# Optimization experiments

Hardware: AMD Instinct MI355X
Metric: run time of the kernel (lower is better)

## Reference

```python
import jax, jax.numpy as jnp
import numpy as np

P, Q, R, H1, H2, PH, B = 32, 32, 8, 128, 64, 16, 8192
PAIRS = P * Q
OUT = PAIRS * R  # X_Z_layer output units


def _pairwise_mask(p, q, r):
    # rows i*q+k correspond to pair (x_i, z_k): connected to x_i and z_k only
    mx = np.zeros((p * q, p), np.float32)
    for i in range(p):
        mx[i * q:(i + 1) * q, i] = 1.0
    mz = np.tile(np.eye(q, dtype=np.float32), (p, 1))
    m = np.concatenate([mx, mz], axis=1)          # [p*q, p+q]
    return np.repeat(m, r, axis=0)                 # [p*q*r, p+q]


def setup_inputs() -> dict:
    key = jax.random.key(0)
    ks = jax.random.split(key, 24)
    rn = lambda k, s, sc=0.1: jax.random.normal(k, s, jnp.float32) * sc
    x = jax.random.normal(ks[0], (B, P), jnp.float32)
    z = jax.random.normal(ks[1], (B, Q), jnp.float32)
    # X_mlp: P -> H1 -> H2 -> 1
    xw1, xb1 = rn(ks[2], (P, H1)), rn(ks[3], (H1,))
    xw2, xb2 = rn(ks[4], (H1, H2)), rn(ks[5], (H2,))
    xw3, xb3 = rn(ks[6], (H2, 1)), rn(ks[7], (1,))
    # Z_mlp: Q -> H1 -> H2 -> 1
    zw1, zb1 = rn(ks[8], (Q, H1)), rn(ks[9], (H1,))
    zw2, zb2 = rn(ks[10], (Q if False else H1, H2)), rn(ks[11], (H2,))
    zw3, zb3 = rn(ks[12], (H2, 1)), rn(ks[13], (1,))
    # masked X_Z_layer: weight pre-multiplied by structured mask (as in __init__)
    mask = jnp.asarray(_pairwise_mask(P, Q, R))    # [OUT, P+Q]
    xzw = (rn(ks[14], (OUT, P + Q)) * mask).T      # [P+Q, OUT]
    xzb = rn(ks[15], (OUT,))
    # 1024 tiny per-pair MLPs: R -> PH (bias) -> 1 (no bias), stacked
    pw1 = rn(ks[16], (PAIRS, R, PH))
    pb1 = rn(ks[17], (PAIRS, PH))
    pw2 = rn(ks[18], (PAIRS, PH))
    return dict(x=x, z=z, xw1=xw1, xb1=xb1, xw2=xw2, xb2=xb2, xw3=xw3, xb3=xb3,
                zw1=zw1, zb1=zb1, zw2=zw2, zb2=zb2, zw3=zw3, zb3=zb3,
                xzw=xzw, xzb=xzb, pw1=pw1, pb1=pb1, pw2=pw2)


def reference(x, z, xw1, xb1, xw2, xb2, xw3, xb3,
              zw1, zb1, zw2, zb2, zw3, zb3, xzw, xzb, pw1, pb1, pw2):
    relu = jax.nn.relu
    # main-effect MLPs
    hx = relu(relu(x @ xw1 + xb1) @ xw2 + xb2)
    out_x = hx @ xw3 + xb3                         # [B,1]
    hz = relu(relu(z @ zw1 + zb1) @ zw2 + zb2)
    out_z = hz @ zw3 + zb3                         # [B,1]
    # masked interaction layer
    xz = jnp.concatenate([x, z], axis=1)           # [B, P+Q]
    h = relu(xz @ xzw + xzb)                       # [B, OUT]
    # all 1024 per-pair MLPs as one batched GEMM
    hp = h.reshape(h.shape[0], PAIRS, R)           # [B, pairs, R]
    t = relu(jnp.einsum('bpr,prh->bph', hp, pw1) + pb1)
    out_xz = jnp.einsum('bph,ph->b', t, pw2)[:, None]  # sum over pairs -> [B,1]
    return out_x + out_z + out_xz
```

## Files before the change

### kernel.cpp

```cpp
#include <hip/hip_runtime.h>

#define B_TOT 8192
#define PP 32
#define QQ 32
#define RR 8
#define H1 128
#define H2 64
#define PHH 16
#define PAIRS 1024
#define OUT_UNITS 8192

#define NBLK_IA 4096
#define NBLK_MM 512

typedef float f32x16 __attribute__((ext_vector_type(16)));
typedef short s16x8  __attribute__((ext_vector_type(8)));

union FragU { s16x8 v; unsigned int u[4]; };

__device__ inline unsigned int pack_bf16(float lo, float hi) {
    return __builtin_amdgcn_perm(__float_as_uint(hi), __float_as_uint(lo), 0x07060302u);
}

union SharedU {
    union {
        struct {
            float zT[16][128];
            float4 lwx[16][2];
            float4 lwz[16][2];
            float4 lhb[16][2];
            unsigned lpw1[16][4][16];
            float lpb[16][16];
            float lpw2[16][16];
        } s;
        float red[128][33];
    } ia;
    struct {
        float h1T[64][65];
        float red2[4][64];
    } mm;
};

__global__ __launch_bounds__(256, 4) void fused_k(
    const float* __restrict__ x, const float* __restrict__ z,
    const float* __restrict__ xw1, const float* __restrict__ xb1,
    const float* __restrict__ xw2, const float* __restrict__ xb2,
    const float* __restrict__ xw3, const float* __restrict__ xb3,
    const float* __restrict__ zw1, const float* __restrict__ zb1,
    const float* __restrict__ zw2, const float* __restrict__ zb2,
    const float* __restrict__ zw3, const float* __restrict__ zb3,
    const float* __restrict__ xzw, const float* __restrict__ xzb,
    const float* __restrict__ pw1, const float* __restrict__ pb1,
    const float* __restrict__ pw2, float* __restrict__ out)
{
    __shared__ SharedU sh;
    const int bid  = blockIdx.x;
    const int t    = threadIdx.x;
    const int w    = t >> 6;
    const int lane = t & 63;

    if (bid >= NBLK_MM) {
        const int ib    = bid - NBLK_MM;
        const int bx    = ib & 63;
        const int y     = ib >> 6;
        const int m     = lane & 31;
        const int kh    = lane >> 5;
        const int jj    = m & 15;
        const int cph   = m >> 4;
        const int b0    = bx * 128;
        const int i_x   = y >> 1;
        const int k0    = (y & 1) * 16;
        const int pair0 = y * 16;

        {
            int row = t >> 1;
            int c8  = (t & 1) * 8;
            const float* src = z + (size_t)(b0 + row) * 32 + k0 + c8;
            float4 a4 = *reinterpret_cast<const float4*>(src);
            float4 b4 = *reinterpret_cast<const float4*>(src + 4);
            sh.ia.s.zT[c8+0][row] = a4.x; sh.ia.s.zT[c8+1][row] = a4.y;
            sh.ia.s.zT[c8+2][row] = a4.z; sh.ia.s.zT[c8+3][row] = a4.w;
            sh.ia.s.zT[c8+4][row] = b4.x; sh.ia.s.zT[c8+5][row] = b4.y;
            sh.ia.s.zT[c8+6][row] = b4.z; sh.ia.s.zT[c8+7][row] = b4.w;
        }
        if (t < 128) {
            int p = t >> 3, c = t & 7;
            int gp = pair0 + p;
            reinterpret_cast<float*>(sh.ia.s.lwx)[t] = xzw[(size_t)i_x * OUT_UNITS + gp*8 + c];
            reinterpret_cast<float*>(sh.ia.s.lwz)[t] = xzw[(size_t)(32 + k0 + p) * OUT_UNITS + gp*8 + c];
            reinterpret_cast<float*>(sh.ia.s.lhb)[t] = xzb[gp*8 + c];
        }
        {
            int p = t >> 4, j = t & 15;
            int gp = pair0 + p;
            sh.ia.s.lpb[p][j]  = pb1[gp*PHH + j];
            sh.ia.s.lpw2[p][j] = pw2[gp*PHH + j];
        }
        #pragma unroll
        for (int it = 0; it < 4; ++it) {
            int idx = t + it * 256;
            int p = idx >> 6, u = (idx >> 4) & 3, j = idx & 15;
            int gp = pair0 + p;
            float lo = pw1[(size_t)gp * 128 + (2*u)*16 + j];
            float hi = pw1[(size_t)gp * 128 + (2*u+1)*16 + j];
            sh.ia.s.lpw1[p][u][j] = pack_bf16(lo, hi);
        }

        const int bl = (w & 1) * 64 + m;
        const float xv0 = x[(size_t)(b0 + bl)      * 32 + i_x];
        const float xv1 = x[(size_t)(b0 + bl + 32) * 32 + i_x];
        __syncthreads();

        f32x16 acc0, acc1;
        #pragma unroll
        for (int r = 0; r < 16; ++r) { acc0[r] = 0.f; acc1[r] = 0.f; }

        const bool realB = (kh == cph);
        const int  ppl0  = (w >> 1) * 4;

        #pragma unroll 2
        for (int kk = 0; kk < 4; ++kk) {
            const int ppl = ppl0 + kk;
            const int pAl = 2*ppl + kh;
            const int pBl = 2*ppl + cph;

            const float zv0 = sh.ia.s.zT[pAl][bl];
            const float zv1 = sh.ia.s.zT[pAl][bl + 32];
            const float4 wxa = sh.ia.s.lwx[pAl][0], wxb = sh.ia.s.lwx[pAl][1];
            const float4 wza = sh.ia.s.lwz[pAl][0], wzb = sh.ia.s.lwz[pAl][1];
            const float4 hba = sh.ia.s.lhb[pAl][0], hbb = sh.ia.s.lhb[pAl][1];

            float h0[8], h1v[8];
            h0[0] = fmaxf(fmaf(xv0, wxa.x, fmaf(zv0, wza.x, hba.x)), 0.f);
            h0[1] = fmaxf(fmaf(xv0, wxa.y, fmaf(zv0, wza.y, hba.y)), 0.f);
            h0[2] = fmaxf(fmaf(xv0, wxa.z, fmaf(zv0, wza.z, hba.z)), 0.f);
            h0[3] = fmaxf(fmaf(xv0, wxa.w, fmaf(zv0, wza.w, hba.w)), 0.f);
            h0[4] = fmaxf(fmaf(xv0, wxb.x, fmaf(zv0, wzb.x, hbb.x)), 0.f);
            h0[5] = fmaxf(fmaf(xv0, wxb.y, fmaf(zv0, wzb.y, hbb.y)), 0.f);
            h0[6] = fmaxf(fmaf(xv0, wxb.z, fmaf(zv0, wzb.z, hbb.z)), 0.f);
            h0[7] = fmaxf(fmaf(xv0, wxb.w, fmaf(zv0, wzb.w, hbb.w)), 0.f);
            h1v[0] = fmaxf(fmaf(xv1, wxa.x, fmaf(zv1, wza.x, hba.x)), 0.f);
            h1v[1] = fmaxf(fmaf(xv1, wxa.y, fmaf(zv1, wza.y, hba.y)), 0.f);
            h1v[2] = fmaxf(fmaf(xv1, wxa.z, fmaf(zv1, wza.z, hba.z)), 0.f);
            h1v[3] = fmaxf(fmaf(xv1, wxa.w, fmaf(zv1, wza.w, hba.w)), 0.f);
            h1v[4] = fmaxf(fmaf(xv1, wxb.x, fmaf(zv1, wzb.x, hbb.x)), 0.f);
            h1v[5] = fmaxf(fmaf(xv1, wxb.y, fmaf(zv1, wzb.y, hbb.y)), 0.f);
            h1v[6] = fmaxf(fmaf(xv1, wxb.z, fmaf(zv1, wzb.z, hbb.z)), 0.f);
            h1v[7] = fmaxf(fmaf(xv1, wxb.w, fmaf(zv1, wzb.w, hbb.w)), 0.f);

            FragU a0, a1, bf;
            a0.u[0] = pack_bf16(h0[0], h0[1]);
            a0.u[1] = pack_bf16(h0[2], h0[3]);
            a0.u[2] = pack_bf16(h0[4], h0[5]);
            a0.u[3] = pack_bf16(h0[6], h0[7]);
            a1.u[0] = pack_bf16(h1v[0], h1v[1]);
            a1.u[1] = pack_bf16(h1v[2], h1v[3]);
            a1.u[2] = pack_bf16(h1v[4], h1v[5]);
            a1.u[3] = pack_bf16(h1v[6], h1v[7]);
            bf.u[0] = realB ? sh.ia.s.lpw1[pBl][0][jj] : 0u;
            bf.u[1] = realB ? sh.ia.s.lpw1[pBl][1][jj] : 0u;
            bf.u[2] = realB ? sh.ia.s.lpw1[pBl][2][jj] : 0u;
            bf.u[3] = realB ? sh.ia.s.lpw1[pBl][3][jj] : 0u;

            const float pbv = sh.ia.s.lpb[pBl][jj];
            const float w2v = sh.ia.s.lpw2[pBl][jj];

            f32x16 cpb;
            #pragma unroll
            for (int r = 0; r < 16; ++r) cpb[r] = pbv;

            f32x16 d0 = __builtin_amdgcn_mfma_f32_32x32x16_bf16(a0.v, bf.v, cpb, 0, 0, 0);
            f32x16 d1 = __builtin_amdgcn_mfma_f32_32x32x16_bf16(a1.v, bf.v, cpb, 0, 0, 0);

            #pragma unroll
            for (int r = 0; r < 16; ++r)
                acc0[r] = fmaf(fmaxf(d0[r], 0.f), w2v, acc0[r]);
            #pragma unroll
            for (int r = 0; r < 16; ++r)
                acc1[r] = fmaf(fmaxf(d1[r], 0.f), w2v, acc1[r]);
        }

        __syncthreads();
        const int rb0 = (w & 1) * 64;
        if (w < 2) {
            #pragma unroll
            for (int r = 0; r < 16; ++r) {
                int rowf = (r & 3) + 8 * (r >> 2) + 4 * kh;
                sh.ia.red[rb0 + rowf][m]      = acc0[r];
                sh.ia.red[rb0 + 32 + rowf][m] = acc1[r];
            }
        }
        __syncthreads();
        if (w >= 2) {
            #pragma unroll
            for (int r = 0; r < 16; ++r) {
                int rowf = (r & 3) + 8 * (r >> 2) + 4 * kh;
                sh.ia.red[rb0 + rowf][m]      += acc0[r];
                sh.ia.red[rb0 + 32 + rowf][m] += acc1[r];
            }
        }
        __syncthreads();
        if (t < 128) {
            float s = 0.f;
            #pragma unroll
            for (int c = 0; c < 32; ++c) s += sh.ia.red[t][c];
            atomicAdd(out + b0 + t, s);
        }
    } else {
        const int r2    = bid;
        const int btile = r2 & 127;
        const int hf    = (r2 >> 7) & 1;
        const int which = (r2 >> 8) & 1;
        const float* in = which ? z   : x;
        const float* w1 = which ? zw1 : xw1;
        const float* b1 = which ? zb1 : xb1;
        const float* w2 = which ? zw2 : xw2;
        const float* b2 = which ? zb2 : xb2;
        const float* w3 = which ? zw3 : xw3;
        const float* b3 = which ? zb3 : xb3;

        const int wu = __builtin_amdgcn_readfirstlane(w);
        const int b0 = btile * 64;

        float xr[32];
        const float4* xrp = reinterpret_cast<const float4*>(in + (size_t)(b0 + lane) * 32);
        #pragma unroll
        for (int q = 0; q < 8; ++q) {
            float4 v = xrp[q];
            xr[4*q] = v.x; xr[4*q+1] = v.y; xr[4*q+2] = v.z; xr[4*q+3] = v.w;
        }

        const int n0 = __builtin_amdgcn_readfirstlane(hf*32 + wu*8);
        float h2[8];
        #pragma unroll
        for (int n = 0; n < 8; ++n) h2[n] = b2[n0 + n];

        #pragma unroll
        for (int half = 0; half < 2; ++half) {
            const int j0 = half*64 + wu*16;
            float h1[16];
            #pragma unroll
            for (int j = 0; j < 16; ++j) h1[j] = b1[j0 + j];
            #pragma unroll
            for (int mm = 0; mm < 32; ++mm) {
                float xv = xr[mm];
                #pragma unroll
                for (int j = 0; j < 16; ++j)
                    h1[j] = fmaf(xv, w1[mm*H1 + j0 + j], h1[j]);
            }
            __syncthreads();
            #pragma unroll
            for (int j = 0; j < 16; ++j)
                sh.mm.h1T[wu*16 + j][lane] = fmaxf(h1[j], 0.f);
            __syncthreads();
            #pragma unroll 4
            for (int mm = 0; mm < 64; ++mm) {
                float hv = sh.mm.h1T[mm][lane];
                #pragma unroll
                for (int n = 0; n < 8; ++n)
                    h2[n] = fmaf(hv, w2[(half*64 + mm)*H2 + n0 + n], h2[n]);
            }
        }
        float p = 0.f;
        #pragma unroll
        for (int n = 0; n < 8; ++n)
            p = fmaf(fmaxf(h2[n], 0.f), w3[n0 + n], p);

        sh.mm.red2[wu][lane] = p;
        __syncthreads();
        if (wu == 0) {
            float s = sh.mm.red2[0][lane] + sh.mm.red2[1][lane]
                    + sh.mm.red2[2][lane] + sh.mm.red2[3][lane];
            if (hf == 0) s += b3[0];
            atomicAdd(out + b0 + lane, s);
        }
    }
}

extern "C" void kernel_launch(void* const* d_in, const int* in_sizes, int n_in,
                              void* d_out, int out_size, void* d_ws, size_t ws_size,
                              hipStream_t stream) {
    const float* x   = (const float*)d_in[0];
    const float* z   = (const float*)d_in[1];
    const float* xw1 = (const float*)d_in[2];
    const float* xb1 = (const float*)d_in[3];
    const float* xw2 = (const float*)d_in[4];
    const float* xb2 = (const float*)d_in[5];
    const float* xw3 = (const float*)d_in[6];
    const float* xb3 = (const float*)d_in[7];
    const float* zw1 = (const float*)d_in[8];
    const float* zb1 = (const float*)d_in[9];
    const float* zw2 = (const float*)d_in[10];
    const float* zb2 = (const float*)d_in[11];
    const float* zw3 = (const float*)d_in[12];
    const float* zb3 = (const float*)d_in[13];
    const float* xzw = (const float*)d_in[14];
    const float* xzb = (const float*)d_in[15];
    const float* pw1 = (const float*)d_in[16];
    const float* pb1 = (const float*)d_in[17];
    const float* pw2 = (const float*)d_in[18];
    float* out = (float*)d_out;

    hipMemsetAsync(out, 0, (size_t)out_size * sizeof(float), stream);

    fused_k<<<dim3(NBLK_IA + NBLK_MM), 256, 0, stream>>>(
        x, z, xw1, xb1, xw2, xb2, xw3, xb3,
        zw1, zb1, zw2, zb2, zw3, zb3,
        xzw, xzb, pw1, pb1, pw2, out);
}
```

Baseline: 128.0 us.

## Double block size to 512 threads, halving grid and per-block weight staging

Blocks grow from 256 to 512 threads. Each interaction block now covers 256 batch rows instead of 128 for its 16 pairs, so the per-pair weights staged into shared memory are loaded and bf16-packed half as often. The MLP blocks now compute the whole 128-wide hidden layer in one pass with 8 waves, which removes the split that needed two atomic passes per output row. The pw1 fragment is stored transposed with an extra zero row, so the masked B operand is read without per-element select branches. The trade-off is larger shared memory per block and possibly lower occupancy at 512 threads under the stated launch bounds.

```diff
diff --git a/kernel.cpp b/kernel.cpp
--- a/kernel.cpp
+++ b/kernel.cpp
@@ -10,8 +10,8 @@
 #define PAIRS 1024
 #define OUT_UNITS 8192
 
-#define NBLK_IA 4096
-#define NBLK_MM 512
+#define NBLK_MM 256
+#define NBLK_IA 2048
 
 typedef float f32x16 __attribute__((ext_vector_type(16)));
 typedef short s16x8  __attribute__((ext_vector_type(8)));
@@ -25,23 +25,23 @@
 union SharedU {
     union {
         struct {
-            float zT[16][128];
+            float zT[16][256];
             float4 lwx[16][2];
             float4 lwz[16][2];
             float4 lhb[16][2];
-            unsigned lpw1[16][4][16];
+            unsigned lpw1T[17][16][4];
             float lpb[16][16];
             float lpw2[16][16];
         } s;
-        float red[128][33];
+        float red[256][33];
     } ia;
     struct {
-        float h1T[64][65];
-        float red2[4][64];
+        float h1T[128][65];
+        float red2[8][64];
     } mm;
 };
 
-__global__ __launch_bounds__(256, 4) void fused_k(
+__global__ __launch_bounds__(512, 4) void fused_k(
     const float* __restrict__ x, const float* __restrict__ z,
     const float* __restrict__ xw1, const float* __restrict__ xb1,
     const float* __restrict__ xw2, const float* __restrict__ xb2,
@@ -61,13 +61,13 @@
 
     if (bid >= NBLK_MM) {
         const int ib    = bid - NBLK_MM;
-        const int bx    = ib & 63;
-        const int y     = ib >> 6;
+        const int bx    = ib & 31;
+        const int y     = ib >> 5;
         const int m     = lane & 31;
         const int kh    = lane >> 5;
         const int jj    = m & 15;
         const int cph   = m >> 4;
-        const int b0    = bx * 128;
+        const int b0    = bx * 256;
         const int i_x   = y >> 1;
         const int k0    = (y & 1) * 16;
         const int pair0 = y * 16;
@@ -90,23 +90,26 @@
             reinterpret_cast<float*>(sh.ia.s.lwz)[t] = xzw[(size_t)(32 + k0 + p) * OUT_UNITS + gp*8 + c];
             reinterpret_cast<float*>(sh.ia.s.lhb)[t] = xzb[gp*8 + c];
         }
-        {
+        if (t < 256) {
             int p = t >> 4, j = t & 15;
             int gp = pair0 + p;
             sh.ia.s.lpb[p][j]  = pb1[gp*PHH + j];
             sh.ia.s.lpw2[p][j] = pw2[gp*PHH + j];
         }
         #pragma unroll
-        for (int it = 0; it < 4; ++it) {
-            int idx = t + it * 256;
+        for (int it = 0; it < 2; ++it) {
+            int idx = t + it * 512;
             int p = idx >> 6, u = (idx >> 4) & 3, j = idx & 15;
             int gp = pair0 + p;
             float lo = pw1[(size_t)gp * 128 + (2*u)*16 + j];
             float hi = pw1[(size_t)gp * 128 + (2*u+1)*16 + j];
-            sh.ia.s.lpw1[p][u][j] = pack_bf16(lo, hi);
-        }
-
-        const int bl = (w & 1) * 64 + m;
+            sh.ia.s.lpw1T[p][j][u] = pack_bf16(lo, hi);
+        }
+        if (t < 64) reinterpret_cast<unsigned*>(sh.ia.s.lpw1T[16])[t] = 0u;
+
+        const int g   = w >> 1;
+        const int pph = w & 1;
+        const int bl  = g * 64 + m;
         const float xv0 = x[(size_t)(b0 + bl)      * 32 + i_x];
         const float xv1 = x[(size_t)(b0 + bl + 32) * 32 + i_x];
         __syncthreads();
@@ -116,11 +119,10 @@
         for (int r = 0; r < 16; ++r) { acc0[r] = 0.f; acc1[r] = 0.f; }
 
         const bool realB = (kh == cph);
-        const int  ppl0  = (w >> 1) * 4;
 
         #pragma unroll 2
         for (int kk = 0; kk < 4; ++kk) {
-            const int ppl = ppl0 + kk;
+            const int ppl = pph * 4 + kk;
             const int pAl = 2*ppl + kh;
             const int pBl = 2*ppl + cph;
 
@@ -157,10 +159,9 @@
             a1.u[1] = pack_bf16(h1v[2], h1v[3]);
             a1.u[2] = pack_bf16(h1v[4], h1v[5]);
             a1.u[3] = pack_bf16(h1v[6], h1v[7]);
-            bf.u[0] = realB ? sh.ia.s.lpw1[pBl][0][jj] : 0u;
-            bf.u[1] = realB ? sh.ia.s.lpw1[pBl][1][jj] : 0u;
-            bf.u[2] = realB ? sh.ia.s.lpw1[pBl][2][jj] : 0u;
-            bf.u[3] = realB ? sh.ia.s.lpw1[pBl][3][jj] : 0u;
+
+            const unsigned* bq = sh.ia.s.lpw1T[realB ? pBl : 16][jj];
+            bf.u[0] = bq[0]; bf.u[1] = bq[1]; bf.u[2] = bq[2]; bf.u[3] = bq[3];
 
             const float pbv = sh.ia.s.lpb[pBl][jj];
             const float w2v = sh.ia.s.lpw2[pBl][jj];
@@ -181,36 +182,34 @@
         }
 
         __syncthreads();
-        const int rb0 = (w & 1) * 64;
-        if (w < 2) {
+        const int rbase = g * 64;
+        if (pph == 0) {
             #pragma unroll
             for (int r = 0; r < 16; ++r) {
                 int rowf = (r & 3) + 8 * (r >> 2) + 4 * kh;
-                sh.ia.red[rb0 + rowf][m]      = acc0[r];
-                sh.ia.red[rb0 + 32 + rowf][m] = acc1[r];
+                sh.ia.red[rbase + rowf][m]      = acc0[r];
+                sh.ia.red[rbase + 32 + rowf][m] = acc1[r];
             }
         }
         __syncthreads();
-        if (w >= 2) {
+        if (pph == 1) {
             #pragma unroll
             for (int r = 0; r < 16; ++r) {
                 int rowf = (r & 3) + 8 * (r >> 2) + 4 * kh;
-                sh.ia.red[rb0 + rowf][m]      += acc0[r];
-                sh.ia.red[rb0 + 32 + rowf][m] += acc1[r];
+                sh.ia.red[rbase + rowf][m]      += acc0[r];
+                sh.ia.red[rbase + 32 + rowf][m] += acc1[r];
             }
         }
         __syncthreads();
-        if (t < 128) {
+        if (t < 256) {
             float s = 0.f;
             #pragma unroll
             for (int c = 0; c < 32; ++c) s += sh.ia.red[t][c];
             atomicAdd(out + b0 + t, s);
         }
     } else {
-        const int r2    = bid;
-        const int btile = r2 & 127;
-        const int hf    = (r2 >> 7) & 1;
-        const int which = (r2 >> 8) & 1;
+        const int btile = bid & 127;
+        const int which = bid >> 7;
         const float* in = which ? z   : x;
         const float* w1 = which ? zw1 : xw1;
         const float* b1 = which ? zb1 : xb1;
@@ -230,36 +229,32 @@
             xr[4*q] = v.x; xr[4*q+1] = v.y; xr[4*q+2] = v.z; xr[4*q+3] = v.w;
         }
 
-        const int n0 = __builtin_amdgcn_readfirstlane(hf*32 + wu*8);
+        const int j0 = wu * 16;
+        float h1[16];
+        #pragma unroll
+        for (int j = 0; j < 16; ++j) h1[j] = b1[j0 + j];
+        #pragma unroll
+        for (int mm = 0; mm < 32; ++mm) {
+            float xv = xr[mm];
+            #pragma unroll
+            for (int j = 0; j < 16; ++j)
+                h1[j] = fmaf(xv, w1[mm*H1 + j0 + j], h1[j]);
+        }
+        #pragma unroll
+        for (int j = 0; j < 16; ++j)
+            sh.mm.h1T[j0 + j][lane] = fmaxf(h1[j], 0.f);
+        __syncthreads();
+
+        const int n0 = __builtin_amdgcn_readfirstlane(wu * 8);
         float h2[8];
         #pragma unroll
         for (int n = 0; n < 8; ++n) h2[n] = b2[n0 + n];
-
-        #pragma unroll
-        for (int half = 0; half < 2; ++half) {
-            const int j0 = half*64 + wu*16;
-            float h1[16];
-            #pragma unroll
-            for (int j = 0; j < 16; ++j) h1[j] = b1[j0 + j];
-            #pragma unroll
-            for (int mm = 0; mm < 32; ++mm) {
-                float xv = xr[mm];
-                #pragma unroll
-                for (int j = 0; j < 16; ++j)
-                    h1[j] = fmaf(xv, w1[mm*H1 + j0 + j], h1[j]);
-            }
-            __syncthreads();
-            #pragma unroll
-            for (int j = 0; j < 16; ++j)
-                sh.mm.h1T[wu*16 + j][lane] = fmaxf(h1[j], 0.f);
-            __syncthreads();
-            #pragma unroll 4
-            for (int mm = 0; mm < 64; ++mm) {
-                float hv = sh.mm.h1T[mm][lane];
-                #pragma unroll
-                for (int n = 0; n < 8; ++n)
-                    h2[n] = fmaf(hv, w2[(half*64 + mm)*H2 + n0 + n], h2[n]);
-            }
+        #pragma unroll 4
+        for (int mm = 0; mm < 128; ++mm) {
+            float hv = sh.mm.h1T[mm][lane];
+            #pragma unroll
+            for (int n = 0; n < 8; ++n)
+                h2[n] = fmaf(hv, w2[mm*H2 + n0 + n], h2[n]);
         }
         float p = 0.f;
         #pragma unroll
@@ -268,11 +263,11 @@
 
         sh.mm.red2[wu][lane] = p;
         __syncthreads();
-        if (wu == 0) {
-            float s = sh.mm.red2[0][lane] + sh.mm.red2[1][lane]
-                    + sh.mm.red2[2][lane] + sh.mm.red2[3][lane];
-            if (hf == 0) s += b3[0];
-            atomicAdd(out + b0 + lane, s);
+        if (t < 64) {
+            float s = b3[0];
+            #pragma unroll
+            for (int ww = 0; ww < 8; ++ww) s += sh.mm.red2[ww][t];
+            atomicAdd(out + b0 + t, s);
         }
     }
 }
@@ -303,7 +298,7 @@
 
     hipMemsetAsync(out, 0, (size_t)out_size * sizeof(float), stream);
 
-    fused_k<<<dim3(NBLK_IA + NBLK_MM), 256, 0, stream>>>(
+    fused_k<<<dim3(NBLK_MM + NBLK_IA), 512, 0, stream>>>(
         x, z, xw1, xb1, xw2, xb2, xw3, xb3,
         zw1, zb1, zw2, zb2, zw3, zb3,
         xzw, xzb, pw1, pb1, pw2, out);
```

New measurement: 130.1 us. About the same (+1.7%).
